# Kernel optimization log

Measured on AMD Instinct MI355X. Metric: run time of the kernel, lower is better.

Reference implementation:

```python
import jax, jax.numpy as jnp
import numpy as np

TOUT = 4096  # fixed padded output frame length (>= max possible cumsum of durations)


def setup_inputs() -> dict:
    key = jax.random.key(0)
    k1, k2 = jax.random.split(key)
    xs = jax.random.normal(k1, (8, 512, 384), dtype=jnp.float32)
    ds = jax.random.randint(k2, (8, 512), 0, 8, dtype=jnp.int64)
    return {"xs": xs, "ds": ds}


def reference(xs, ds):
    # xs: (B, Tin, D) phoneme embeddings; ds: (B, Tin) integer durations.
    # Build mapping matrix M: (B, Tout, Tin) where M[b, t, i] = 1 iff frame t
    # falls in [cumsum(ds)[i] - ds[i], cumsum(ds)[i]), then ys = M @ xs.
    cum = jnp.cumsum(ds, axis=1)          # (B, Tin) right boundaries
    left = cum - ds                        # (B, Tin) left boundaries
    frames = jnp.arange(TOUT)              # (Tout,)
    f = frames[None, :, None]              # (1, Tout, 1)
    M = ((f >= left[:, None, :]) & (f < cum[:, None, :])).astype(xs.dtype)  # (B, Tout, Tin)
    ys = jnp.einsum('bti,bid->btd', M, xs)  # (B, Tout, D)
    return ys
```

## Files before the change

### kernel.cpp

```cpp
#include <hip/hip_runtime.h>

#define NB    8
#define NIN   512
#define TOUT  4096
#define ND    384
#define J4    (ND / 4)
#define TROWS 16
#define BLK   256

typedef float f32x4 __attribute__((ext_vector_type(4)));

__global__ __launch_bounds__(BLK) void lenreg(const f32x4* __restrict__ xs,
                                              const int* __restrict__ ds,
                                              f32x4* __restrict__ out) {
    const int b       = blockIdx.x & 7;
    const int rowbase = (blockIdx.x >> 3) * TROWS;
    const int tid     = threadIdx.x;

    __shared__ int cum[NIN];
    __shared__ int wsum[BLK / 64];
    __shared__ int owner[TROWS];

    const int* dsb = ds + b * NIN;
    const int a0 = dsb[2 * tid];
    const int a1 = dsb[2 * tid + 1];
    int p = a0 + a1;
    const int lane = tid & 63;
    const int wid  = tid >> 6;
    #pragma unroll
    for (int off = 1; off < 64; off <<= 1) {
        int v = __shfl_up(p, off, 64);
        if (lane >= off) p += v;
    }
    if (lane == 63) wsum[wid] = p;
    __syncthreads();
    int acc = 0;
    #pragma unroll
    for (int w = 0; w < BLK / 64; ++w)
        if (w < wid) acc += wsum[w];
    p += acc;
    cum[2 * tid + 1] = p;
    cum[2 * tid]     = p - a1;
    __syncthreads();

    const int total = cum[NIN - 1];
    if (tid < TROWS) {
        const int t = rowbase + tid;
        int o = -1;
        if (t < total) {
            int lo = 0, hi = NIN;
            #pragma unroll
            for (int s = 0; s < 10; ++s) {
                if (lo < hi) {
                    int mid = (lo + hi) >> 1;
                    if (cum[mid] > t) hi = mid; else lo = mid + 1;
                }
            }
            o = lo;
        }
        owner[tid] = o;
    }
    __syncthreads();

    const f32x4* xsb  = xs + (size_t)b * NIN * J4;
    f32x4*       outb = out + ((size_t)b * TOUT + rowbase) * J4;
    constexpr int ITER = TROWS * J4 / BLK;
    f32x4 v[ITER];
    #pragma unroll
    for (int k = 0; k < ITER; ++k) {
        const int g = k * BLK + tid;
        const int o = owner[g / J4];
        v[k] = (f32x4)(0.f);
        if (o >= 0) v[k] = xsb[o * J4 + (g - (g / J4) * J4)];
    }
    #pragma unroll
    for (int k = 0; k < ITER; ++k)
        outb[k * BLK + tid] = v[k];
}

extern "C" void kernel_launch(void* const* d_in, const int* in_sizes, int n_in,
                              void* d_out, int out_size, void* d_ws, size_t ws_size,
                              hipStream_t stream) {
    const float* xs = (const float*)d_in[0];
    const int*   ds = (const int*)d_in[1];
    float* out = (float*)d_out;

    lenreg<<<(TOUT / TROWS) * NB, BLK, 0, stream>>>((const f32x4*)xs, ds,
                                                    (f32x4*)out);
}
```

Baseline: 74.95 us.

## Split owner-map construction into a prepass kernel and use nontemporal stores

The per-block prefix sum and binary search are replaced by a small kernel that builds a per-frame owner index in workspace once per batch, and a gather kernel that reads owner indices from global memory. Redundant scans in each of the 2048 blocks are removed, at the cost of an extra launch and a dependency between kernels. Output writes switch to nontemporal stores to avoid polluting cache with streaming data.

Measured after the change: 77.44 us. 1.03x slower.

```diff
diff --git a/kernel.cpp b/kernel.cpp
--- a/kernel.cpp
+++ b/kernel.cpp
@@ -10,16 +10,12 @@
 
 typedef float f32x4 __attribute__((ext_vector_type(4)));
 
-__global__ __launch_bounds__(BLK) void lenreg(const f32x4* __restrict__ xs,
-                                              const int* __restrict__ ds,
-                                              f32x4* __restrict__ out) {
-    const int b       = blockIdx.x & 7;
-    const int rowbase = (blockIdx.x >> 3) * TROWS;
-    const int tid     = threadIdx.x;
-
-    __shared__ int cum[NIN];
+__global__ __launch_bounds__(BLK) void build_owner(const int* __restrict__ ds,
+                                                   int* __restrict__ owner) {
+    const int b   = blockIdx.x;
+    const int tid = threadIdx.x;
     __shared__ int wsum[BLK / 64];
-    __shared__ int owner[TROWS];
+    __shared__ int s_total;
 
     const int* dsb = ds + b * NIN;
     const int a0 = dsb[2 * tid];
@@ -39,43 +35,48 @@
     for (int w = 0; w < BLK / 64; ++w)
         if (w < wid) acc += wsum[w];
     p += acc;
-    cum[2 * tid + 1] = p;
-    cum[2 * tid]     = p - a1;
+
+    if (tid == BLK - 1) s_total = p;
+
+    int* ob = owner + b * TOUT;
+    const int incl1 = p;
+    const int incl0 = p - a1;
+    const int left0 = incl0 - a0;
+    for (int f = left0; f < incl0; ++f) ob[f] = 2 * tid;
+    for (int f = incl0; f < incl1; ++f) ob[f] = 2 * tid + 1;
     __syncthreads();
+    for (int f = s_total + tid; f < TOUT; f += BLK) ob[f] = -1;
+}
 
-    const int total = cum[NIN - 1];
-    if (tid < TROWS) {
-        const int t = rowbase + tid;
-        int o = -1;
-        if (t < total) {
-            int lo = 0, hi = NIN;
-            #pragma unroll
-            for (int s = 0; s < 10; ++s) {
-                if (lo < hi) {
-                    int mid = (lo + hi) >> 1;
-                    if (cum[mid] > t) hi = mid; else lo = mid + 1;
-                }
-            }
-            o = lo;
-        }
-        owner[tid] = o;
-    }
-    __syncthreads();
+__global__ __launch_bounds__(BLK) void gather(const f32x4* __restrict__ xs,
+                                              const int* __restrict__ owner,
+                                              f32x4* __restrict__ out) {
+    const int b       = blockIdx.x & 7;
+    const int rowbase = (blockIdx.x >> 3) * TROWS;
+    const int tid     = threadIdx.x;
 
+    const int*   ob   = owner + b * TOUT + rowbase;
     const f32x4* xsb  = xs + (size_t)b * NIN * J4;
     f32x4*       outb = out + ((size_t)b * TOUT + rowbase) * J4;
+
     constexpr int ITER = TROWS * J4 / BLK;
+    int o[ITER], col[ITER];
+    #pragma unroll
+    for (int k = 0; k < ITER; ++k) {
+        const int g = k * BLK + tid;
+        const int r = g / J4;
+        col[k] = g - r * J4;
+        o[k]   = ob[r];
+    }
     f32x4 v[ITER];
     #pragma unroll
     for (int k = 0; k < ITER; ++k) {
-        const int g = k * BLK + tid;
-        const int o = owner[g / J4];
         v[k] = (f32x4)(0.f);
-        if (o >= 0) v[k] = xsb[o * J4 + (g - (g / J4) * J4)];
+        if (o[k] >= 0) v[k] = xsb[o[k] * J4 + col[k]];
     }
     #pragma unroll
     for (int k = 0; k < ITER; ++k)
-        outb[k * BLK + tid] = v[k];
+        __builtin_nontemporal_store(v[k], &outb[k * BLK + tid]);
 }
 
 extern "C" void kernel_launch(void* const* d_in, const int* in_sizes, int n_in,
@@ -84,7 +85,9 @@
     const float* xs = (const float*)d_in[0];
     const int*   ds = (const int*)d_in[1];
     float* out = (float*)d_out;
+    int*   owner = (int*)d_ws;
 
-    lenreg<<<(TOUT / TROWS) * NB, BLK, 0, stream>>>((const f32x4*)xs, ds,
+    build_owner<<<NB, BLK, 0, stream>>>(ds, owner);
+    gather<<<(TOUT / TROWS) * NB, BLK, 0, stream>>>((const f32x4*)xs, owner,
                                                     (f32x4*)out);
 }
```
